# Optimization experiments

Measured on AMD Instinct MI355X. Metric: run time of the kernel, lower is better.

## Reference

```python
import jax, jax.numpy as jnp
import numpy as np

T = 0.07          # temperature
K_POS = 5         # top-k positives per noun and for mask prediction
MARGIN = 0.1
LAM_CONTRAST = 0.6
LAM_MASK = 0.4


def _l2n(x):
    return x / jnp.linalg.norm(x, axis=-1, keepdims=True)


def setup_inputs() -> dict:
    key = jax.random.key(0)
    k0, k1, k2, k3 = jax.random.split(key, 4)
    B, N, D, M = 64, 576, 512, 16  # N = 24*24 patch grid
    patch_feats = _l2n(jax.random.normal(k0, (B, N, D), jnp.float32))
    noun_feats = _l2n(jax.random.normal(k1, (B, M, D), jnp.float32))
    global_img_feat = _l2n(jax.random.normal(k2, (B, D), jnp.float32))
    global_txt_feat = _l2n(jax.random.normal(k3, (B, D), jnp.float32))
    logit_scale = jnp.full((1,), 1.0 / 0.07, jnp.float32)
    idx = jnp.arange(B, dtype=jnp.int32)
    return {
        "patch_feats": patch_feats,
        "noun_feats": noun_feats,
        "global_img_feat": global_img_feat,
        "global_txt_feat": global_txt_feat,
        "logit_scale": logit_scale,
        "idx": idx,
    }


def _fine_grained_loss(patch_feats, noun_feats):
    # sim[b,m,n] = <noun_m, patch_n>; replaces the nested Python loops.
    B = patch_feats.shape[0]
    sim = jnp.einsum('bmd,bnd->bmn', noun_feats, patch_feats)
    scaled = sim / T
    # Per-noun contrastive loss. log_softmax over cat([topk, rest]) equals
    # log_softmax over all N entries evaluated at the topk positions, so:
    #   loss = -sum_topk log_softmax = K_POS*lse - sum(topk scaled values)
    lse = jax.nn.logsumexp(scaled, axis=-1)              # [B, M]
    topv, _ = jax.lax.top_k(scaled, K_POS)               # [B, M, K]
    contrast_loss = jnp.mean(K_POS * lse - topv.sum(-1))
    # Mask-prediction BCE loss (pool_type='mean').
    pooled = sim.mean(axis=1)                            # [B, N]
    _, tidx = jax.lax.top_k(pooled, K_POS)               # [B, K]
    pred = jnp.zeros_like(pooled).at[jnp.arange(B)[:, None], tidx].set(1.0)
    x = pooled / T
    mask_loss = jnp.mean(jnp.logaddexp(0.0, x) - x * pred)
    return LAM_CONTRAST * contrast_loss + LAM_MASK * mask_loss


def _contrastive_loss(img, txt, logit_scale, idx):
    logits = logit_scale.reshape(()) * (img @ txt.T)
    pos = (idx[:, None] == idx[None, :]).astype(logits.dtype)
    labels = pos / pos.sum(axis=1, keepdims=True)
    li2t = -(jax.nn.log_softmax(logits, axis=1) * labels).sum(1).mean()
    lt2i = -(jax.nn.log_softmax(logits.T, axis=1) * labels).sum(1).mean()
    return 0.5 * (li2t + lt2i)


def _triplet_loss(img, txt):
    scores = img @ txt.T
    d = jnp.diagonal(scores)
    eye = jnp.eye(scores.shape[0], dtype=bool)
    cost_s = jnp.where(eye, 0.0, jnp.clip(MARGIN + scores - d[:, None], 0.0)).sum()
    cost_im = jnp.where(eye, 0.0, jnp.clip(MARGIN + scores - d[None, :], 0.0)).sum()
    return 0.5 * (cost_s + cost_im)


def reference(patch_feats, noun_feats, global_img_feat, global_txt_feat, logit_scale, idx):
    loss_c = _contrastive_loss(global_img_feat, global_txt_feat, logit_scale, idx)
    loss_t = _triplet_loss(global_img_feat, global_txt_feat)
    loss_f = _fine_grained_loss(patch_feats, noun_feats)
    return jnp.stack([loss_c, loss_t, loss_f])
```

## Files before the change

kernel.cpp:

```cpp
#include <hip/hip_runtime.h>
#include <hip/hip_bf16.h>
#include <math.h>

#define NB 64
#define NN 576
#define ND 512
#define NM 16
#define QPB 9
#define KPOS 5
#define TINV 14.2857142857142857f

#define NFINE (NB * QPB * 2)
#define NBLK1 (NFINE + NB)
#define WS_SIM 4096
#define LSTR 33

#define FINF __builtin_inff()

__device__ __forceinline__ void ins5(float (&a)[5], float v) {
  if (v > a[4]) {
    a[4] = v;
    if (a[4] > a[3]) { float x = a[4]; a[4] = a[3]; a[3] = x; }
    if (a[3] > a[2]) { float x = a[3]; a[3] = a[2]; a[2] = x; }
    if (a[2] > a[1]) { float x = a[2]; a[2] = a[1]; a[1] = x; }
    if (a[1] > a[0]) { float x = a[1]; a[1] = a[0]; a[0] = x; }
  }
}

__device__ __forceinline__ void merge5(float (&a)[5], const float (&b)[5]) {
  float r[5];
#pragma unroll
  for (int k = 0; k < 5; ++k) {
    float best = -FINF;
#pragma unroll
    for (int i = 0; i <= k + 1; ++i) {
      const int j = k + 1 - i;
      const float av = (i == 0) ? FINF : a[i - 1];
      const float bv = (j == 0) ? FINF : b[j - 1];
      best = fmaxf(best, fminf(av, bv));
    }
    r[k] = best;
  }
#pragma unroll
  for (int k = 0; k < 5; ++k) a[k] = r[k];
}

__device__ __forceinline__ void merge5_shfl(float (&a)[5], int msk) {
  float o[5];
#pragma unroll
  for (int k = 0; k < 5; ++k) o[k] = __shfl_xor(a[k], msk, 64);
  merge5(a, o);
}

__global__ __launch_bounds__(256) void k_sim(
    const float* __restrict__ patch, const float* __restrict__ noun,
    const float* __restrict__ gimg, const float* __restrict__ gtxt,
    float* __restrict__ ws) {
  const int blk = blockIdx.x;
  const int t = threadIdx.x;
  const int lane = t & 63;

  __shared__ float L[4 * 64 * LSTR];

  if (blk < NFINE) {
    const int bq = blk >> 1, h = blk & 1;
    const int b = bq / QPB, quad = bq - b * QPB;
    const int wv = __builtin_amdgcn_readfirstlane(t >> 6);
    const int d0 = h * 256 + wv * 64;

    const float* pbase = patch + ((size_t)(b * NN + quad * 64)) * ND + d0;
    const float* nbase = noun + (size_t)b * NM * ND + d0;
    float* WP = &L[wv * (64 * LSTR)];

    const int sp = lane >> 3;
    const int sf = lane & 7;

    float acc[NM];
#pragma unroll
    for (int m = 0; m < NM; ++m) acc[m] = 0.f;

    float4 stg[8];
#pragma unroll
    for (int r = 0; r < 8; ++r)
      stg[r] = *(const float4*)(pbase + (size_t)(8 * r + sp) * ND + sf * 4);

#pragma unroll
    for (int c = 0; c < 2; ++c) {
      __syncthreads();
#pragma unroll
      for (int r = 0; r < 8; ++r) {
        float* dst = &WP[(8 * r + sp) * LSTR + sf * 4];
        dst[0] = stg[r].x; dst[1] = stg[r].y; dst[2] = stg[r].z; dst[3] = stg[r].w;
      }
      __syncthreads();
      if (c == 0) {
#pragma unroll
        for (int r = 0; r < 8; ++r)
          stg[r] = *(const float4*)(pbase + 32 + (size_t)(8 * r + sp) * ND + sf * 4);
      }
      float pf[32];
#pragma unroll
      for (int d = 0; d < 32; ++d) pf[d] = WP[lane * LSTR + d];
      const float* nc = nbase + c * 32;
#pragma unroll 4
      for (int m = 0; m < NM; ++m) {
        const float* np_ = nc + m * ND;
        float s0 = 0.f, s1 = 0.f;
#pragma unroll
        for (int d = 0; d < 32; d += 2) {
          s0 += pf[d] * np_[d];
          s1 += pf[d + 1] * np_[d + 1];
        }
        acc[m] += s0 + s1;
      }
    }

    __syncthreads();
#pragma unroll
    for (int m = 0; m < NM; ++m) L[wv * 1024 + m * 64 + lane] = acc[m];
    __syncthreads();
    float* dst = ws + WS_SIM + (size_t)blk * 1024;
    for (int i = t; i < 1024; i += 256)
      dst[i] = L[i] + L[1024 + i] + L[2048 + i] + L[3072 + i];
  } else {
    const int i = blk - NFINE;
    const int dq = t >> 6;
    const float4* ip = (const float4*)(gimg + (size_t)i * ND + dq * 128);
    const float4* tp = (const float4*)(gtxt + (size_t)lane * ND + dq * 128);
    float a = 0.f;
#pragma unroll
    for (int q = 0; q < 32; ++q) {
      const float4 x = ip[q];
      const float4 y = tp[q];
      a += x.x * y.x + x.y * y.y + x.z * y.z + x.w * y.w;
    }
    L[dq * 64 + lane] = a;
    __syncthreads();
    if (t < 64) ws[i * 64 + t] = L[t] + L[64 + t] + L[128 + t] + L[192 + t];
  }
}

__global__ __launch_bounds__(256) void k_loss(
    const float* __restrict__ ws, const float* __restrict__ lscale,
    const int* __restrict__ idx, float* __restrict__ out) {
  const int blk = blockIdx.x;
  const int t = threadIdx.x;
  const int lane = t & 63;
  const int w = t >> 6;

  __shared__ float S[NM * 577 + 64];

  if (blk < NB) {
    const int b = blk;
#pragma unroll
    for (int q = 0; q < QPB; ++q) {
      const float4* t0 = (const float4*)(ws + WS_SIM + ((size_t)(b * QPB + q) * 2 + 0) * 1024);
      const float4* t1 = (const float4*)(ws + WS_SIM + ((size_t)(b * QPB + q) * 2 + 1) * 1024);
      const float4 a = t0[t];
      const float4 c = t1[t];
      const int i0 = 4 * t;
      const int m = i0 >> 6, p = i0 & 63;
      float* dst = &S[m * 577 + q * 64 + p];
      dst[0] = (a.x + c.x) * TINV;
      dst[1] = (a.y + c.y) * TINV;
      dst[2] = (a.z + c.z) * TINV;
      dst[3] = (a.w + c.w) * TINV;
    }
    __syncthreads();

    float cpart = 0.f;
#pragma unroll
    for (int mi = 0; mi < 4; ++mi) {
      const int m = w * 4 + mi;
      const float* row = &S[m * 577];
      float mx = -FINF;
#pragma unroll
      for (int k = 0; k < 9; ++k) mx = fmaxf(mx, row[lane + 64 * k]);
#pragma unroll
      for (int msk = 1; msk < 64; msk <<= 1) mx = fmaxf(mx, __shfl_xor(mx, msk, 64));
      float se = 0.f;
      float t5[5] = {-FINF, -FINF, -FINF, -FINF, -FINF};
#pragma unroll
      for (int k = 0; k < 9; ++k) {
        const float v = row[lane + 64 * k];
        se += expf(v - mx);
        ins5(t5, v);
      }
#pragma unroll
      for (int msk = 1; msk < 64; msk <<= 1) {
        se += __shfl_xor(se, msk, 64);
        merge5_shfl(t5, msk);
      }
      if (lane == 0) {
        const float st = t5[0] + t5[1] + t5[2] + t5[3] + t5[4];
        cpart += (KPOS * (mx + logf(se)) - st) * (0.6f / (float)(NB * NM));
      }
    }

    float sxp = 0.f;
    float u5[5] = {-FINF, -FINF, -FINF, -FINF, -FINF};
#pragma unroll
    for (int rep = 0; rep < 3; ++rep) {
      const int n = t + rep * 256;
      if (n < NN) {
        float cs = 0.f;
#pragma unroll
        for (int m = 0; m < NM; ++m) cs += S[m * 577 + n];
        const float x = cs * (1.f / 16.f);
        sxp += (x > 0.f) ? (x + log1pf(expf(-x))) : log1pf(expf(x));
        ins5(u5, x);
      }
    }
#pragma unroll
    for (int msk = 1; msk < 64; msk <<= 1) {
      sxp += __shfl_xor(sxp, msk, 64);
      merge5_shfl(u5, msk);
    }
    float* R = &S[NM * 577];
    if (lane == 0) {
      R[w] = cpart;
      R[8 + w] = sxp;
#pragma unroll
      for (int k = 0; k < 5; ++k) R[16 + w * 5 + k] = u5[k];
    }
    __syncthreads();
    if (t == 0) {
      float tot = R[0] + R[1] + R[2] + R[3];
      float sp = R[8] + R[9] + R[10] + R[11];
      float f5[5] = {R[16], R[17], R[18], R[19], R[20]};
#pragma unroll
      for (int ww = 1; ww < 4; ++ww) {
        float o[5] = {R[16 + ww * 5], R[17 + ww * 5], R[18 + ww * 5],
                      R[19 + ww * 5], R[20 + ww * 5]};
        merge5(f5, o);
      }
      const float st = f5[0] + f5[1] + f5[2] + f5[3] + f5[4];
      tot += (sp - st) * (0.4f / (float)(NB * NN));
      atomicAdd(out + 2, tot);
    }
    return;
  }

  float* S_ = &S[0];
  for (int i = t; i < 4096; i += 256) S_[(i >> 6) * 65 + (i & 63)] = ws[i];
  __syncthreads();
  float* dgp = &S[4160];
  int* idl = (int*)&S[4224];
  if (t < 64) { dgp[t] = S_[t * 66]; idl[t] = idx[t]; }
  __syncthreads();
  if (t < 64) {
    const float sc = lscale[0];
    float mR = -FINF, mC = -FINF;
    for (int j = 0; j < 64; ++j) {
      mR = fmaxf(mR, sc * S_[t * 65 + j]);
      mC = fmaxf(mC, sc * S_[j * 65 + t]);
    }
    float seR = 0.f, seC = 0.f;
    for (int j = 0; j < 64; ++j) {
      seR += expf(sc * S_[t * 65 + j] - mR);
      seC += expf(sc * S_[j * 65 + t] - mC);
    }
    const float lseR = mR + logf(seR);
    const float lseC = mC + logf(seC);
    const int myid = idl[t];
    const float di = dgp[t];
    float ps = 0.f, trow = 0.f, tcol = 0.f, cs = 0.f, ci = 0.f;
    for (int j = 0; j < 64; ++j) {
      const float sv = S_[t * 65 + j];
      const float svT = S_[j * 65 + t];
      if (idl[j] == myid) {
        ps += 1.f;
        trow += sc * sv - lseR;
        tcol += sc * svT - lseC;
      }
      if (j != t) {
        cs += fmaxf(0.f, 0.1f + sv - di);
        ci += fmaxf(0.f, 0.1f + sv - dgp[j]);
      }
    }
    float vc = -(trow + tcol) / ps;
    float vt = cs + ci;
#pragma unroll
    for (int msk = 1; msk < 64; msk <<= 1) {
      vc += __shfl_xor(vc, msk, 64);
      vt += __shfl_xor(vt, msk, 64);
    }
    if (t == 0) {
      out[0] = vc * (0.5f / 64.f);
      out[1] = vt * 0.5f;
    }
  }
}

extern "C" void kernel_launch(void* const* d_in, const int* in_sizes, int n_in,
                              void* d_out, int out_size, void* d_ws, size_t ws_size,
                              hipStream_t stream) {
  const float* patch = (const float*)d_in[0];
  const float* noun  = (const float*)d_in[1];
  const float* gimg  = (const float*)d_in[2];
  const float* gtxt  = (const float*)d_in[3];
  const float* lsc   = (const float*)d_in[4];
  const int*   idx   = (const int*)d_in[5];
  float* out = (float*)d_out;
  float* ws  = (float*)d_ws;

  hipMemsetAsync(d_out, 0, 3 * sizeof(float), stream);
  k_sim<<<dim3(NBLK1), dim3(256), 0, stream>>>(patch, noun, gimg, gtxt, ws);
  k_loss<<<dim3(NB + 1), dim3(256), 0, stream>>>(ws, lsc, idx, out);
}
```

Baseline: 149.5 us.

## Compute noun-patch similarities with bf16 MFMA instead of fp32 FMA

Replaces the fp32 FMA dot-product path with 16x16x32 bf16 MFMA. Each wave converts noun and patch rows to bf16 on the fly and accumulates a 16x16 tile over the full D. It also drops the split-D halving, which removes the LDS staging and the reduction of partial sums in the loss kernel. The cost is bf16 rounding of inputs, which can perturb top-k selection and the loss values.

```diff
diff --git a/kernel.cpp b/kernel.cpp
--- a/kernel.cpp
+++ b/kernel.cpp
@@ -10,12 +10,27 @@
 #define KPOS 5
 #define TINV 14.2857142857142857f
 
-#define NFINE (NB * QPB * 2)
+#define NFINE (NB * QPB)
 #define NBLK1 (NFINE + NB)
 #define WS_SIM 4096
-#define LSTR 33
 
 #define FINF __builtin_inff()
+
+typedef __attribute__((ext_vector_type(8))) short short8;
+typedef __attribute__((ext_vector_type(4))) float floatx4;
+
+__device__ __forceinline__ short f2bf(float f) {
+  unsigned u = __float_as_uint(f);
+  u += 0x7FFFu + ((u >> 16) & 1u);
+  return (short)(u >> 16);
+}
+
+__device__ __forceinline__ short8 pack8(const float4 a, const float4 b) {
+  short8 r;
+  r[0] = f2bf(a.x); r[1] = f2bf(a.y); r[2] = f2bf(a.z); r[3] = f2bf(a.w);
+  r[4] = f2bf(b.x); r[5] = f2bf(b.y); r[6] = f2bf(b.z); r[7] = f2bf(b.w);
+  return r;
+}
 
 __device__ __forceinline__ void ins5(float (&a)[5], float v) {
   if (v > a[4]) {
@@ -60,68 +75,35 @@
   const int t = threadIdx.x;
   const int lane = t & 63;
 
-  __shared__ float L[4 * 64 * LSTR];
+  __shared__ float L[256];
 
   if (blk < NFINE) {
-    const int bq = blk >> 1, h = blk & 1;
-    const int b = bq / QPB, quad = bq - b * QPB;
-    const int wv = __builtin_amdgcn_readfirstlane(t >> 6);
-    const int d0 = h * 256 + wv * 64;
-
-    const float* pbase = patch + ((size_t)(b * NN + quad * 64)) * ND + d0;
-    const float* nbase = noun + (size_t)b * NM * ND + d0;
-    float* WP = &L[wv * (64 * LSTR)];
-
-    const int sp = lane >> 3;
-    const int sf = lane & 7;
-
-    float acc[NM];
-#pragma unroll
-    for (int m = 0; m < NM; ++m) acc[m] = 0.f;
-
-    float4 stg[8];
-#pragma unroll
-    for (int r = 0; r < 8; ++r)
-      stg[r] = *(const float4*)(pbase + (size_t)(8 * r + sp) * ND + sf * 4);
-
-#pragma unroll
-    for (int c = 0; c < 2; ++c) {
-      __syncthreads();
-#pragma unroll
-      for (int r = 0; r < 8; ++r) {
-        float* dst = &WP[(8 * r + sp) * LSTR + sf * 4];
-        dst[0] = stg[r].x; dst[1] = stg[r].y; dst[2] = stg[r].z; dst[3] = stg[r].w;
-      }
-      __syncthreads();
-      if (c == 0) {
-#pragma unroll
-        for (int r = 0; r < 8; ++r)
-          stg[r] = *(const float4*)(pbase + 32 + (size_t)(8 * r + sp) * ND + sf * 4);
-      }
-      float pf[32];
-#pragma unroll
-      for (int d = 0; d < 32; ++d) pf[d] = WP[lane * LSTR + d];
-      const float* nc = nbase + c * 32;
-#pragma unroll 4
-      for (int m = 0; m < NM; ++m) {
-        const float* np_ = nc + m * ND;
-        float s0 = 0.f, s1 = 0.f;
-#pragma unroll
-        for (int d = 0; d < 32; d += 2) {
-          s0 += pf[d] * np_[d];
-          s1 += pf[d + 1] * np_[d + 1];
-        }
-        acc[m] += s0 + s1;
-      }
-    }
-
-    __syncthreads();
-#pragma unroll
-    for (int m = 0; m < NM; ++m) L[wv * 1024 + m * 64 + lane] = acc[m];
-    __syncthreads();
+    const int b = blk / QPB, quad = blk - b * QPB;
+    const int w = t >> 6;
+    const int nidx = lane & 15;
+    const int k0 = (lane >> 4) * 8;
+
+    const float* nrow = noun + ((size_t)b * NM + nidx) * ND + k0;
+    const float* prow = patch + ((size_t)(b * NN + quad * 64 + w * 16 + nidx)) * ND + k0;
+
+    floatx4 acc = {0.f, 0.f, 0.f, 0.f};
+#pragma unroll
+    for (int ks = 0; ks < 16; ++ks) {
+      const int o = ks * 32;
+      const float4 a0 = *(const float4*)(nrow + o);
+      const float4 a1 = *(const float4*)(nrow + o + 4);
+      const float4 p0 = *(const float4*)(prow + o);
+      const float4 p1 = *(const float4*)(prow + o + 4);
+      const short8 af = pack8(a0, a1);
+      const short8 bf = pack8(p0, p1);
+      acc = __builtin_amdgcn_mfma_f32_16x16x32_bf16(af, bf, acc, 0, 0, 0);
+    }
+
     float* dst = ws + WS_SIM + (size_t)blk * 1024;
-    for (int i = t; i < 1024; i += 256)
-      dst[i] = L[i] + L[1024 + i] + L[2048 + i] + L[3072 + i];
+    const int mrow = (lane >> 4) * 4;
+    const int pcol = w * 16 + nidx;
+#pragma unroll
+    for (int r = 0; r < 4; ++r) dst[(mrow + r) * 64 + pcol] = acc[r];
   } else {
     const int i = blk - NFINE;
     const int dq = t >> 6;
@@ -154,17 +136,15 @@
     const int b = blk;
 #pragma unroll
     for (int q = 0; q < QPB; ++q) {
-      const float4* t0 = (const float4*)(ws + WS_SIM + ((size_t)(b * QPB + q) * 2 + 0) * 1024);
-      const float4* t1 = (const float4*)(ws + WS_SIM + ((size_t)(b * QPB + q) * 2 + 1) * 1024);
+      const float4* t0 = (const float4*)(ws + WS_SIM + (size_t)(b * QPB + q) * 1024);
       const float4 a = t0[t];
-      const float4 c = t1[t];
       const int i0 = 4 * t;
       const int m = i0 >> 6, p = i0 & 63;
       float* dst = &S[m * 577 + q * 64 + p];
-      dst[0] = (a.x + c.x) * TINV;
-      dst[1] = (a.y + c.y) * TINV;
-      dst[2] = (a.z + c.z) * TINV;
-      dst[3] = (a.w + c.w) * TINV;
+      dst[0] = a.x * TINV;
+      dst[1] = a.y * TINV;
+      dst[2] = a.z * TINV;
+      dst[3] = a.w * TINV;
     }
     __syncthreads();
 
```

Result: faster. 140.6 us (-6.0%).
